# Optimization experiments

Hardware: AMD Instinct MI355X
Metric: run time of the kernel (lower is better)

Reference implementation:

```python
import jax, jax.numpy as jnp
import numpy as np
import math

B, S, E, H = 2, 2048, 1024, 16
D = E // H  # d_head = 64

def setup_inputs() -> dict:
    key = jax.random.key(0)
    ks = jax.random.split(key, 7)
    query = jax.random.normal(ks[0], (B, S, E), dtype=jnp.float32)
    k_in = jax.random.normal(ks[1], (B, S, E), dtype=jnp.float32)
    v_in = jax.random.normal(ks[2], (B, S, E), dtype=jnp.float32)
    # causal mask, broadcastable over batch and heads; mask==0 positions are blocked
    mask = jnp.tril(jnp.ones((S, S), dtype=jnp.int32))[None, None]
    scale = 1.0 / math.sqrt(E)
    w_q = jax.random.normal(ks[3], (E, E), dtype=jnp.float32) * scale
    w_k = jax.random.normal(ks[4], (E, E), dtype=jnp.float32) * scale
    w_v = jax.random.normal(ks[5], (E, E), dtype=jnp.float32) * scale
    w_o = jax.random.normal(ks[6], (E, E), dtype=jnp.float32) * scale
    return {"query": query, "key": k_in, "value": v_in, "mask": mask,
            "w_q": w_q, "w_k": w_k, "w_v": w_v, "w_o": w_o}

def reference(query, key, value, mask, w_q, w_k, w_v, w_o):
    # projections (nn.Linear with no bias: x @ W^T); split heads -> [B,H,S,D]
    q = (query @ w_q.T).reshape(B, S, H, D).transpose(0, 2, 1, 3)
    k = (key @ w_k.T).reshape(B, S, H, D).transpose(0, 2, 1, 3)
    v = (value @ w_v.T).reshape(B, S, H, D).transpose(0, 2, 1, 3)
    # scaled dot-product scores [B,H,S,S]
    scores = jnp.einsum('bhqd,bhkd->bhqk', q, k) / math.sqrt(D)
    scores = jnp.where(mask == 0, jnp.float32(-1e9), scores)
    attn = jax.nn.softmax(scores, axis=-1)  # dropout p=0.0 -> identity
    out = jnp.einsum('bhqk,bhkd->bhqd', attn, v)  # [B,H,S,D]
    out = out.transpose(0, 2, 1, 3).reshape(B, S, E)
    return out @ w_o.T
```

## Files before the change

kernel.cpp:

```cpp
#include <hip/hip_runtime.h>
#include <hip/hip_bf16.h>

#define B_ 2
#define S_ 2048
#define E_ 1024
#define H_ 16
#define D_ 64

typedef __attribute__((ext_vector_type(8))) short bf16x8;
typedef __attribute__((ext_vector_type(4))) float f32x4;

static __device__ __forceinline__ unsigned short f2bf(float x) {
    union { float f; unsigned u; } v; v.f = x;
    unsigned r = v.u + 0x7FFF + ((v.u >> 16) & 1);
    return (unsigned short)(r >> 16);
}

static __device__ __forceinline__ unsigned pack2bf(float a, float b) {
    union { float f; unsigned u; } x, y; x.f = a; y.f = b;
    unsigned ra = x.u + 0x7FFF + ((x.u >> 16) & 1);
    unsigned rb = y.u + 0x7FFF + ((y.u >> 16) & 1);
    return (ra >> 16) | (rb & 0xFFFF0000u);
}

static __device__ __forceinline__ unsigned packtrunc(float a, float b) {
    union { float f; unsigned u; } x, y; x.f = a; y.f = b;
    return __builtin_amdgcn_perm(y.u, x.u, 0x07060302);
}

static __device__ __forceinline__ void async_copy16(const void* gsrc, void* ldst) {
    __builtin_amdgcn_global_load_lds(
        (const __attribute__((address_space(1))) void*)gsrc,
        (__attribute__((address_space(3))) void*)ldst, 16, 0, 0);
}

__global__ void cvt_multi(const float* __restrict__ s0, const float* __restrict__ s1,
                          const float* __restrict__ s2, const float* __restrict__ s3,
                          unsigned short* __restrict__ dst, int n4,
                          float c0, float c1, float c2, float c3) {
    const float* src = (blockIdx.y == 0) ? s0 : (blockIdx.y == 1) ? s1
                     : (blockIdx.y == 2) ? s2 : s3;
    float c = (blockIdx.y == 0) ? c0 : (blockIdx.y == 1) ? c1
            : (blockIdx.y == 2) ? c2 : c3;
    int i = blockIdx.x * blockDim.x + threadIdx.x;
    if (i >= n4) return;
    float4 f = ((const float4*)src)[i];
    ushort4 o;
    o.x = f2bf(f.x * c); o.y = f2bf(f.y * c); o.z = f2bf(f.z * c); o.w = f2bf(f.w * c);
    ((ushort4*)(dst + (size_t)blockIdx.y * n4 * 4))[i] = o;
}

template <int MODE>
__global__ __launch_bounds__(256) void gemm128(
    const unsigned short* __restrict__ A0, const unsigned short* __restrict__ B0,
    void* __restrict__ C0, int M, int N, int K) {
    __shared__ __align__(16) unsigned short Al[2][128 * 64];
    __shared__ __align__(16) unsigned short Bl[2][128 * 64];
    const unsigned short* A = A0;
    const unsigned short* Bm = B0;
    int z = 0;
    if (MODE == 4) {
        z = blockIdx.z;
        A  = A0 + (size_t)z * 4194304;
        Bm = B0 + (size_t)z * 1048576;
    }
    const int bm = blockIdx.y * 128, bn = blockIdx.x * 128;
    const int tid = threadIdx.x;
    const int w = tid >> 6, lane = tid & 63;
    const int col = lane & 15, quad = lane >> 4, swz = col & 7;
    const int wm = (w >> 1) * 64, wn = (w & 1) * 64;

    f32x4 acc[4][4] = {};

#pragma unroll
    for (int it = 0; it < 4; it++) {
        int s = tid + it * 256, r = s >> 3, cg = (s & 7) ^ (r & 7);
        async_copy16(A + (size_t)(bm + r) * K + cg * 8, &Al[0][s * 8]);
        async_copy16(Bm + (size_t)(bn + r) * K + cg * 8, &Bl[0][s * 8]);
    }

    const int nk = K >> 6;
    for (int kt = 0; kt < nk; kt++) {
        const int cur = kt & 1;
        __syncthreads();
        if (kt + 1 < nk) {
            const int k1 = (kt + 1) << 6, nb = cur ^ 1;
#pragma unroll
            for (int it = 0; it < 4; it++) {
                int s = tid + it * 256, r = s >> 3, cg = (s & 7) ^ (r & 7);
                async_copy16(A + (size_t)(bm + r) * K + k1 + cg * 8, &Al[nb][s * 8]);
                async_copy16(Bm + (size_t)(bn + r) * K + k1 + cg * 8, &Bl[nb][s * 8]);
            }
        }
        const unsigned short* Ab = &Al[cur][0];
        const unsigned short* Bb = &Bl[cur][0];
#pragma unroll
        for (int h = 0; h < 2; h++) {
            const int cq = ((h * 4 + quad) ^ swz) * 8;
            bf16x8 af[4], bf[4];
#pragma unroll
            for (int i = 0; i < 4; i++) af[i] = *(const bf16x8*)&Ab[(wm + i * 16 + col) * 64 + cq];
#pragma unroll
            for (int j = 0; j < 4; j++) bf[j] = *(const bf16x8*)&Bb[(wn + j * 16 + col) * 64 + cq];
#pragma unroll
            for (int i = 0; i < 4; i++)
#pragma unroll
                for (int j = 0; j < 4; j++)
                    acc[i][j] = __builtin_amdgcn_mfma_f32_16x16x32_bf16(af[i], bf[j], acc[i][j], 0, 0, 0);
        }
    }

    if (MODE == 3) {
#pragma unroll
        for (int i = 0; i < 4; i++)
#pragma unroll
            for (int j = 0; j < 4; j++)
#pragma unroll
                for (int r = 0; r < 4; r++) {
                    int gm = bm + wm + i * 16 + quad * 4 + r;
                    int gn = bn + wn + j * 16 + col;
                    ((float*)C0)[(size_t)gm * N + gn] = acc[i][j][r];
                }
    } else {
        __syncthreads();
        unsigned short* scr = ((w < 2) ? &Al[0][0] : &Bl[0][0]) + (w & 1) * 4096;
        const int b  = (bm + wm) >> 11;
        const int s0 = (bm + wm) & 2047;
        const int hh = (bn + wn) >> 6;
        unsigned short* outp = (unsigned short*)C0 + (size_t)z * 4194304;
        if (z == 2) {
#pragma unroll
            for (int i = 0; i < 4; i++)
#pragma unroll
                for (int j = 0; j < 4; j++) {
                    int n = j * 16 + col;
                    int c = i * 2 + (quad >> 1);
                    uint2 pk;
                    pk.x = pack2bf(acc[i][j][0], acc[i][j][1]);
                    pk.y = pack2bf(acc[i][j][2], acc[i][j][3]);
                    *(uint2*)&scr[n * 64 + ((c ^ (n & 7)) << 3) + ((quad & 1) << 2)] = pk;
                }
#pragma unroll
            for (int it = 0; it < 8; it++) {
                int slot = it * 64 + lane, n = slot >> 3, c = slot & 7;
                uint4 v = *(uint4*)&scr[n * 64 + ((c ^ (n & 7)) << 3)];
                *(uint4*)&outp[(((size_t)b * H_ + hh) * D_ + n) * S_ + s0 + c * 8] = v;
            }
        } else {
#pragma unroll
            for (int i = 0; i < 4; i++)
#pragma unroll
                for (int j = 0; j < 4; j++)
#pragma unroll
                    for (int r = 0; r < 4; r++) {
                        int m = i * 16 + quad * 4 + r, n = j * 16 + col;
                        scr[m * 64 + (((n >> 3) ^ (m & 7)) << 3) + (n & 7)] = f2bf(acc[i][j][r]);
                    }
#pragma unroll
            for (int it = 0; it < 8; it++) {
                int slot = it * 64 + lane, m = slot >> 3, c = slot & 7;
                uint4 v = *(uint4*)&scr[m * 64 + ((c ^ (m & 7)) << 3)];
                *(uint4*)&outp[(((size_t)b * H_ + hh) * S_ + s0 + m) * (size_t)D_ + c * 8] = v;
            }
        }
    }
}

__global__ __launch_bounds__(256) void attn_kernel(
    const unsigned short* __restrict__ Q, const unsigned short* __restrict__ K_,
    const unsigned short* __restrict__ Vt, unsigned short* __restrict__ Out) {
    __shared__ __align__(16) unsigned short Kl[2][64 * 64];
    __shared__ __align__(16) unsigned short Vl[2][64 * 64];
    const int bh = blockIdx.y;
    const int qb = (bh >= 16) ? (int)blockIdx.x : 15 - (int)blockIdx.x;
    const int q0 = qb * 128;
    const int tid = threadIdx.x;
    const int w = tid >> 6, lane = tid & 63;
    const int col = lane & 15, quad = lane >> 4, swz = col & 7;
    const int qw0 = q0 + w * 32;
    const float NINF = -__builtin_huge_valf();

    const unsigned short* Qh = Q + (size_t)bh * S_ * D_;
    const unsigned short* Kh = K_ + (size_t)bh * S_ * D_;
    const unsigned short* Vh = Vt + (size_t)bh * D_ * S_;

    bf16x8 qf[2][2];
#pragma unroll
    for (int i = 0; i < 2; i++)
#pragma unroll
        for (int h = 0; h < 2; h++)
            qf[i][h] = *(const bf16x8*)(Qh + (size_t)(qw0 + i * 16 + col) * 64 + h * 32 + quad * 8);

    f32x4 o[2][4] = {};
    float lsum[2] = {0.f, 0.f};

#pragma unroll
    for (int it = 0; it < 2; it++) {
        int s = tid + it * 256, r = s >> 3, cg = (s & 7) ^ (r & 7);
        async_copy16(Kh + (size_t)r * 64 + cg * 8, &Kl[0][s * 8]);
        async_copy16(Vh + (size_t)r * S_ + cg * 8, &Vl[0][s * 8]);
    }

    const int nk = 2 * (qb + 1);
    for (int kt = 0; kt < nk; kt++) {
        const int k0 = kt * 64;
        const int cur = kt & 1;
        __syncthreads();
        if (kt + 1 < nk) {
            const int k1 = k0 + 64, nb = cur ^ 1;
#pragma unroll
            for (int it = 0; it < 2; it++) {
                int s = tid + it * 256, r = s >> 3, cg = (s & 7) ^ (r & 7);
                async_copy16(Kh + (size_t)(k1 + r) * 64 + cg * 8, &Kl[nb][s * 8]);
                async_copy16(Vh + (size_t)r * S_ + k1 + cg * 8, &Vl[nb][s * 8]);
            }
        }
        if (k0 > qw0 + 31) continue;

        const unsigned short* Kb = &Kl[cur][0];
        const unsigned short* Vb = &Vl[cur][0];

        f32x4 sc[2][4] = {};
#pragma unroll
        for (int h = 0; h < 2; h++) {
            const int cq = ((h * 4 + quad) ^ swz) * 8;
#pragma unroll
            for (int ct = 0; ct < 4; ct++) {
                bf16x8 kf = *(const bf16x8*)&Kb[(ct * 16 + col) * 64 + cq];
                sc[0][ct] = __builtin_amdgcn_mfma_f32_16x16x32_bf16(kf, qf[0][h], sc[0][ct], 0, 0, 0);
                sc[1][ct] = __builtin_amdgcn_mfma_f32_16x16x32_bf16(kf, qf[1][h], sc[1][ct], 0, 0, 0);
            }
        }
        if (k0 + 63 <= qw0) {
#pragma unroll
            for (int i = 0; i < 2; i++)
#pragma unroll
                for (int ct = 0; ct < 4; ct++) {
#pragma unroll
                    for (int r = 0; r < 4; r++)
                        sc[i][ct][r] = __builtin_amdgcn_exp2f(sc[i][ct][r]);
                    lsum[i] += (sc[i][ct][0] + sc[i][ct][1]) + (sc[i][ct][2] + sc[i][ct][3]);
                }
        } else {
#pragma unroll
            for (int i = 0; i < 2; i++)
#pragma unroll
                for (int ct = 0; ct < 4; ct++) {
#pragma unroll
                    for (int r = 0; r < 4; r++) {
                        int key = k0 + ct * 16 + quad * 4 + r;
                        int qi = qw0 + i * 16 + col;
                        float s = (key <= qi) ? sc[i][ct][r] : NINF;
                        sc[i][ct][r] = __builtin_amdgcn_exp2f(s);
                    }
                    lsum[i] += (sc[i][ct][0] + sc[i][ct][1]) + (sc[i][ct][2] + sc[i][ct][3]);
                }
        }
        union { bf16x8 v; unsigned u[4]; } pf[2][2];
#pragma unroll
        for (int i = 0; i < 2; i++)
#pragma unroll
            for (int kh = 0; kh < 2; kh++) {
                pf[i][kh].u[0] = packtrunc(sc[i][2 * kh][0], sc[i][2 * kh][1]);
                pf[i][kh].u[1] = packtrunc(sc[i][2 * kh][2], sc[i][2 * kh][3]);
                pf[i][kh].u[2] = packtrunc(sc[i][2 * kh + 1][0], sc[i][2 * kh + 1][1]);
                pf[i][kh].u[3] = packtrunc(sc[i][2 * kh + 1][2], sc[i][2 * kh + 1][3]);
            }
#pragma unroll
        for (int kh = 0; kh < 2; kh++)
#pragma unroll
            for (int dt = 0; dt < 4; dt++) {
                const int row = dt * 16 + col;
                const int ko0 = kh * 32 + quad * 4;
                const int ko1 = ko0 + 16;
                union { bf16x8 v; uint2 d2[2]; } vf;
                vf.d2[0] = *(const uint2*)&Vb[row * 64 + (((ko0 >> 3) ^ (row & 7)) << 3) + (ko0 & 7)];
                vf.d2[1] = *(const uint2*)&Vb[row * 64 + (((ko1 >> 3) ^ (row & 7)) << 3) + (ko1 & 7)];
#pragma unroll
                for (int i = 0; i < 2; i++)
                    o[i][dt] = __builtin_amdgcn_mfma_f32_16x16x32_bf16(vf.v, pf[i][kh].v, o[i][dt], 0, 0, 0);
            }
    }

    const int b = bh >> 4, hh = bh & 15;
#pragma unroll
    for (int i = 0; i < 2; i++) {
        float l = lsum[i];
        l += __shfl_xor(l, 16);
        l += __shfl_xor(l, 32);
        float inv = 1.f / l;
        int gq = qw0 + i * 16 + col;
#pragma unroll
        for (int dt = 0; dt < 4; dt++) {
            uint2 pk;
            pk.x = pack2bf(o[i][dt][0] * inv, o[i][dt][1] * inv);
            pk.y = pack2bf(o[i][dt][2] * inv, o[i][dt][3] * inv);
            *(uint2*)&Out[((size_t)b * S_ + gq) * E_ + hh * 64 + dt * 16 + quad * 4] = pk;
        }
    }
}

extern "C" void kernel_launch(void* const* d_in, const int* in_sizes, int n_in,
                              void* d_out, int out_size, void* d_ws, size_t ws_size,
                              hipStream_t stream) {
    const float* query = (const float*)d_in[0];
    const float* key_i = (const float*)d_in[1];
    const float* value = (const float*)d_in[2];
    const float* w_q = (const float*)d_in[4];
    const float* w_k = (const float*)d_in[5];
    const float* w_v = (const float*)d_in[6];
    const float* w_o = (const float*)d_in[7];
    float* out = (float*)d_out;

    const int M = B_ * S_;
    const int N = E_, K = E_;
    const size_t nX = (size_t)M * E_;
    const size_t nW = (size_t)E_ * E_;

    char* ws = (char*)d_ws;
    unsigned short* xq  = (unsigned short*)(ws);
    unsigned short* wqb = (unsigned short*)(ws + (24u << 20));
    unsigned short* Qb  = (unsigned short*)(ws + (32u << 20));
    unsigned short* Kb  = (unsigned short*)(ws + (40u << 20));
    unsigned short* Vtb = (unsigned short*)(ws + (48u << 20));
    unsigned short* Ab  = (unsigned short*)(ws + (56u << 20));

    const float SCQ = 0.125f * 1.44269504088896f;

    int n4x = (int)(nX / 4), n4w = (int)(nW / 4);
    cvt_multi<<<dim3((n4x + 255) / 256, 3), 256, 0, stream>>>(
        query, key_i, value, value, xq, n4x, 1.f, 1.f, 1.f, 1.f);
    cvt_multi<<<dim3((n4w + 255) / 256, 4), 256, 0, stream>>>(
        w_q, w_k, w_v, w_o, wqb, n4w, SCQ, 1.f, 1.f, 1.f);

    gemm128<4><<<dim3(N / 128, M / 128, 3), 256, 0, stream>>>(xq, wqb, Qb, M, N, K);

    attn_kernel<<<dim3(S_ / 128, B_ * H_), 256, 0, stream>>>(Qb, Kb, Vtb, Ab);

    gemm128<3><<<dim3(N / 128, M / 128), 256, 0, stream>>>(
        Ab, wqb + 3u * 1048576u, out, M, N, K);
}
```

Before: 232.5 us.

## Split attention key tiles across two waves per query group with LDS reduction

The attention block grows from 4 to 8 waves. Each pair of waves shares a 32-row query group and each wave handles one 32-key half of every 64-key tile. Partial output accumulators and row sums from the second wave go through LDS, reusing the K/V buffers after a barrier, and are added into the first wave before normalisation and store. The aim is more waves in flight and shorter per-wave dependency chains for this small grid of 512 blocks. The cost is an extra reduction step and barriers, and each wave now issues fewer MFMAs per loaded tile.

```diff
diff --git a/kernel.cpp b/kernel.cpp
--- a/kernel.cpp
+++ b/kernel.cpp
@@ -166,18 +166,19 @@
     }
 }
 
-__global__ __launch_bounds__(256) void attn_kernel(
+__global__ __launch_bounds__(512) void attn_kernel(
     const unsigned short* __restrict__ Q, const unsigned short* __restrict__ K_,
     const unsigned short* __restrict__ Vt, unsigned short* __restrict__ Out) {
-    __shared__ __align__(16) unsigned short Kl[2][64 * 64];
-    __shared__ __align__(16) unsigned short Vl[2][64 * 64];
+    __shared__ __align__(16) unsigned short KV[4][4096];
+    __shared__ __align__(16) float Lred[4][2][64];
     const int bh = blockIdx.y;
     const int qb = (bh >= 16) ? (int)blockIdx.x : 15 - (int)blockIdx.x;
     const int q0 = qb * 128;
     const int tid = threadIdx.x;
     const int w = tid >> 6, lane = tid & 63;
+    const int qg = w >> 1, kh = w & 1, kh32 = kh << 5;
     const int col = lane & 15, quad = lane >> 4, swz = col & 7;
-    const int qw0 = q0 + w * 32;
+    const int qw0 = q0 + qg * 32;
     const float NINF = -__builtin_huge_valf();
 
     const unsigned short* Qh = Q + (size_t)bh * S_ * D_;
@@ -194,11 +195,10 @@
     f32x4 o[2][4] = {};
     float lsum[2] = {0.f, 0.f};
 
-#pragma unroll
-    for (int it = 0; it < 2; it++) {
-        int s = tid + it * 256, r = s >> 3, cg = (s & 7) ^ (r & 7);
-        async_copy16(Kh + (size_t)r * 64 + cg * 8, &Kl[0][s * 8]);
-        async_copy16(Vh + (size_t)r * S_ + cg * 8, &Vl[0][s * 8]);
+    {
+        int s = tid, r = s >> 3, cg = (s & 7) ^ (r & 7);
+        async_copy16(Kh + (size_t)r * 64 + cg * 8, &KV[0][s * 8]);
+        async_copy16(Vh + (size_t)r * S_ + cg * 8, &KV[2][s * 8]);
     }
 
     const int nk = 2 * (qb + 1);
@@ -208,34 +208,31 @@
         __syncthreads();
         if (kt + 1 < nk) {
             const int k1 = k0 + 64, nb = cur ^ 1;
-#pragma unroll
-            for (int it = 0; it < 2; it++) {
-                int s = tid + it * 256, r = s >> 3, cg = (s & 7) ^ (r & 7);
-                async_copy16(Kh + (size_t)(k1 + r) * 64 + cg * 8, &Kl[nb][s * 8]);
-                async_copy16(Vh + (size_t)r * S_ + k1 + cg * 8, &Vl[nb][s * 8]);
-            }
-        }
-        if (k0 > qw0 + 31) continue;
-
-        const unsigned short* Kb = &Kl[cur][0];
-        const unsigned short* Vb = &Vl[cur][0];
-
-        f32x4 sc[2][4] = {};
+            int s = tid, r = s >> 3, cg = (s & 7) ^ (r & 7);
+            async_copy16(Kh + (size_t)(k1 + r) * 64 + cg * 8, &KV[nb][s * 8]);
+            async_copy16(Vh + (size_t)r * S_ + k1 + cg * 8, &KV[2 + nb][s * 8]);
+        }
+        if (k0 + kh32 > qw0 + 31) continue;
+
+        const unsigned short* Kb = &KV[cur][0];
+        const unsigned short* Vb = &KV[2 + cur][0];
+
+        f32x4 sc[2][2] = {};
 #pragma unroll
         for (int h = 0; h < 2; h++) {
             const int cq = ((h * 4 + quad) ^ swz) * 8;
 #pragma unroll
-            for (int ct = 0; ct < 4; ct++) {
-                bf16x8 kf = *(const bf16x8*)&Kb[(ct * 16 + col) * 64 + cq];
+            for (int ct = 0; ct < 2; ct++) {
+                bf16x8 kf = *(const bf16x8*)&Kb[(kh32 + ct * 16 + col) * 64 + cq];
                 sc[0][ct] = __builtin_amdgcn_mfma_f32_16x16x32_bf16(kf, qf[0][h], sc[0][ct], 0, 0, 0);
                 sc[1][ct] = __builtin_amdgcn_mfma_f32_16x16x32_bf16(kf, qf[1][h], sc[1][ct], 0, 0, 0);
             }
         }
-        if (k0 + 63 <= qw0) {
+        if (k0 + kh32 + 31 <= qw0) {
 #pragma unroll
             for (int i = 0; i < 2; i++)
 #pragma unroll
-                for (int ct = 0; ct < 4; ct++) {
+                for (int ct = 0; ct < 2; ct++) {
 #pragma unroll
                     for (int r = 0; r < 4; r++)
                         sc[i][ct][r] = __builtin_amdgcn_exp2f(sc[i][ct][r]);
@@ -245,10 +242,10 @@
 #pragma unroll
             for (int i = 0; i < 2; i++)
 #pragma unroll
-                for (int ct = 0; ct < 4; ct++) {
+                for (int ct = 0; ct < 2; ct++) {
 #pragma unroll
                     for (int r = 0; r < 4; r++) {
-                        int key = k0 + ct * 16 + quad * 4 + r;
+                        int key = k0 + kh32 + ct * 16 + quad * 4 + r;
                         int qi = qw0 + i * 16 + col;
                         float s = (key <= qi) ? sc[i][ct][r] : NINF;
                         sc[i][ct][r] = __builtin_amdgcn_exp2f(s);
@@ -256,46 +253,63 @@
                     lsum[i] += (sc[i][ct][0] + sc[i][ct][1]) + (sc[i][ct][2] + sc[i][ct][3]);
                 }
         }
-        union { bf16x8 v; unsigned u[4]; } pf[2][2];
+        union { bf16x8 v; unsigned u[4]; } pf[2];
+#pragma unroll
+        for (int i = 0; i < 2; i++) {
+            pf[i].u[0] = packtrunc(sc[i][0][0], sc[i][0][1]);
+            pf[i].u[1] = packtrunc(sc[i][0][2], sc[i][0][3]);
+            pf[i].u[2] = packtrunc(sc[i][1][0], sc[i][1][1]);
+            pf[i].u[3] = packtrunc(sc[i][1][2], sc[i][1][3]);
+        }
+#pragma unroll
+        for (int dt = 0; dt < 4; dt++) {
+            const int row = dt * 16 + col;
+            const int ko0 = kh32 + quad * 4;
+            const int ko1 = ko0 + 16;
+            union { bf16x8 v; uint2 d2[2]; } vf;
+            vf.d2[0] = *(const uint2*)&Vb[row * 64 + (((ko0 >> 3) ^ (row & 7)) << 3) + (ko0 & 7)];
+            vf.d2[1] = *(const uint2*)&Vb[row * 64 + (((ko1 >> 3) ^ (row & 7)) << 3) + (ko1 & 7)];
+#pragma unroll
+            for (int i = 0; i < 2; i++)
+                o[i][dt] = __builtin_amdgcn_mfma_f32_16x16x32_bf16(vf.v, pf[i].v, o[i][dt], 0, 0, 0);
+        }
+    }
+
+    __syncthreads();
+    if (kh == 1) {
+        f32x4* R = (f32x4*)&KV[0][0] + qg * 512 + lane * 8;
 #pragma unroll
         for (int i = 0; i < 2; i++)
 #pragma unroll
-            for (int kh = 0; kh < 2; kh++) {
-                pf[i][kh].u[0] = packtrunc(sc[i][2 * kh][0], sc[i][2 * kh][1]);
-                pf[i][kh].u[1] = packtrunc(sc[i][2 * kh][2], sc[i][2 * kh][3]);
-                pf[i][kh].u[2] = packtrunc(sc[i][2 * kh + 1][0], sc[i][2 * kh + 1][1]);
-                pf[i][kh].u[3] = packtrunc(sc[i][2 * kh + 1][2], sc[i][2 * kh + 1][3]);
-            }
-#pragma unroll
-        for (int kh = 0; kh < 2; kh++)
+            for (int dt = 0; dt < 4; dt++) R[i * 4 + dt] = o[i][dt];
+        Lred[qg][0][lane] = lsum[0];
+        Lred[qg][1][lane] = lsum[1];
+    }
+    __syncthreads();
+    if (kh == 0) {
+        f32x4* R = (f32x4*)&KV[0][0] + qg * 512 + lane * 8;
+#pragma unroll
+        for (int i = 0; i < 2; i++)
+#pragma unroll
+            for (int dt = 0; dt < 4; dt++) o[i][dt] += R[i * 4 + dt];
+        lsum[0] += Lred[qg][0][lane];
+        lsum[1] += Lred[qg][1][lane];
+
+        const int b = bh >> 4, hh = bh & 15;
+#pragma unroll
+        for (int i = 0; i < 2; i++) {
+            float l = lsum[i];
+            l += __shfl_xor(l, 16);
+            l += __shfl_xor(l, 32);
+            float inv = 1.f / l;
+            int gq = qw0 + i * 16 + col;
 #pragma unroll
             for (int dt = 0; dt < 4; dt++) {
-                const int row = dt * 16 + col;
-                const int ko0 = kh * 32 + quad * 4;
-                const int ko1 = ko0 + 16;
-                union { bf16x8 v; uint2 d2[2]; } vf;
-                vf.d2[0] = *(const uint2*)&Vb[row * 64 + (((ko0 >> 3) ^ (row & 7)) << 3) + (ko0 & 7)];
-                vf.d2[1] = *(const uint2*)&Vb[row * 64 + (((ko1 >> 3) ^ (row & 7)) << 3) + (ko1 & 7)];
-#pragma unroll
-                for (int i = 0; i < 2; i++)
-                    o[i][dt] = __builtin_amdgcn_mfma_f32_16x16x32_bf16(vf.v, pf[i][kh].v, o[i][dt], 0, 0, 0);
-            }
-    }
-
-    const int b = bh >> 4, hh = bh & 15;
-#pragma unroll
-    for (int i = 0; i < 2; i++) {
-        float l = lsum[i];
-        l += __shfl_xor(l, 16);
-        l += __shfl_xor(l, 32);
-        float inv = 1.f / l;
-        int gq = qw0 + i * 16 + col;
-#pragma unroll
-        for (int dt = 0; dt < 4; dt++) {
-            uint2 pk;
-            pk.x = pack2bf(o[i][dt][0] * inv, o[i][dt][1] * inv);
-            pk.y = pack2bf(o[i][dt][2] * inv, o[i][dt][3] * inv);
-            *(uint2*)&Out[((size_t)b * S_ + gq) * E_ + hh * 64 + dt * 16 + quad * 4] = pk;
+                uint2 pk;
+                pk.x = pack2bf(o[i][dt][0] * inv, o[i][dt][1] * inv);
+                pk.y = pack2bf(o[i][dt][2] * inv, o[i][dt][3] * inv);
+                *(uint2*)&Out[((size_t)b * S_ + gq) * E_ + hh * 64 + dt * 16 + quad * 4] = pk;
+            }
         }
     }
 }
@@ -335,7 +349,7 @@
 
     gemm128<4><<<dim3(N / 128, M / 128, 3), 256, 0, stream>>>(xq, wqb, Qb, M, N, K);
 
-    attn_kernel<<<dim3(S_ / 128, B_ * H_), 256, 0, stream>>>(Qb, Kb, Vtb, Ab);
+    attn_kernel<<<dim3(S_ / 128, B_ * H_), 512, 0, stream>>>(Qb, Kb, Vtb, Ab);
 
     gemm128<3><<<dim3(N / 128, M / 128), 256, 0, stream>>>(
         Ab, wqb + 3u * 1048576u, out, M, N, K);
```

New measurement: 225.4 us. -3.0%, faster.
